# Kernel tuning notes

Measured on AMD Instinct MI355X. Metric: run time of the kernel, lower is better.

## Reference

```python
import jax, jax.numpy as jnp
import numpy as np

N = 100000   # n_node
D = 100      # emb_size
K = 100      # K1 (channel 0 cluster count)
L = 3        # layers
NNZ = 1600000  # sparse adjacency nnz (avg degree 16)


def _l2norm(x):
    # F.normalize(x, dim=-1, p=2) with eps=1e-12
    return x / jnp.maximum(jnp.linalg.norm(x, axis=-1, keepdims=True), 1e-12)


def setup_inputs() -> dict:
    key = jax.random.key(0)
    ks = jax.random.split(key, 8)
    s = 1.0 / np.sqrt(D)  # module's uniform(-stdv, stdv) init
    embedding = jax.random.normal(ks[0], (N, D), jnp.float32)
    adj = jax.random.uniform(ks[1], (N,), jnp.float32) + 0.01  # per-node positive weights
    edge_rows = jax.random.randint(ks[2], (NNZ,), 0, N, jnp.int32)
    edge_cols = jax.random.randint(ks[3], (NNZ,), 0, N, jnp.int32)
    edge_vals = jax.random.uniform(ks[4], (NNZ,), jnp.float32)
    W_item = jax.random.uniform(ks[5], (L, D, D), jnp.float32, -s, s)
    W_i1 = jax.random.uniform(ks[6], (D, D), jnp.float32, -s, s)
    W_i2 = jax.random.uniform(ks[7], (D, K), jnp.float32, -s, s)
    return {"embedding": embedding, "adj": adj, "edge_vals": edge_vals,
            "W_item": W_item, "W_i1": W_i1, "W_i2": W_i2,
            "edge_rows": edge_rows, "edge_cols": edge_cols}


def reference(embedding, adj, edge_vals, W_item, W_i1, W_i2, edge_rows, edge_cols):
    # ItemConv.forward for one channel (channel=0), adjacency as COO sparse [N,N]
    def spmm(x):  # torch.sparse.mm(adjacency, x)
        return jax.ops.segment_sum(edge_vals[:, None] * x[edge_cols], edge_rows,
                                   num_segments=N)

    x = embedding
    final = [x]
    finalh = []
    for i in range(L):
        x = x @ W_item[i]                       # Linear(D, D, bias=False)
        x = spmm(x)                             # [N, D]
        H1 = jax.nn.relu(x @ W_i1 + x)          # residual + ReLU
        H1 = jax.nn.softmax(H1 @ W_i2, axis=1)  # [N, K] soft cluster assignment
        h = H1.T * adj[None, :]                 # [K, N]
        h = h / jnp.sum(h, axis=0)              # column-normalize over clusters
        h = h @ x                               # [K, D] cluster aggregates
        h = H1 @ h                              # [N, D] redistribute to nodes
        x = h + x                               # residual
        final.append(_l2norm(x))
        finalh.append(_l2norm(h))
    item_embeddings = sum(final) / (L + 1)
    hs = sum(finalh) / L
    return item_embeddings, hs
```

## Files before the change

### kernel.cpp

```cpp
#include <hip/hip_runtime.h>
#include <hip/hip_bf16.h>

#define D 100
#define XS 128

typedef __hip_bfloat16 bf16;
typedef __attribute__((ext_vector_type(8))) short bf16x8;
typedef __attribute__((ext_vector_type(4))) float f32x4;

__device__ __forceinline__ float ldf(const void* p, long long i, int f32) {
    return f32 ? ((const float*)p)[i] : __bfloat162float(((const bf16*)p)[i]);
}

__device__ __forceinline__ float b2f(unsigned short u) {
    return __uint_as_float(((unsigned int)u) << 16);
}

__device__ __forceinline__ unsigned short f2bu(float x) {
    union { bf16 b; unsigned short u; } cv;
    cv.b = __float2bfloat16(x);
    return cv.u;
}

__global__ void detectk(const void* __restrict__ emb, int* __restrict__ flag)
{
    const unsigned short* u = (const unsigned short*)emb;
    __shared__ int cnt;
    if (threadIdx.x == 0) cnt = 0;
    __syncthreads();
    int good = 0;
    for (int i = threadIdx.x; i < 512; i += 256) {
        int e = (u[i] >> 7) & 0xFF;
        if (e >= 118 && e <= 137) good++;
    }
    atomicAdd(&cnt, good);
    __syncthreads();
    if (threadIdx.x == 0) *flag = (cnt >= 410) ? 0 : 1;
}


__global__ void wprep(const void* __restrict__ wi, const void* __restrict__ w1,
    const void* __restrict__ w2, const int* __restrict__ flag,
    bf16* __restrict__ wh, bf16* __restrict__ wl)
{
    int i = blockIdx.x * 256 + threadIdx.x;
    if (i >= 5 * 112 * 128) return;
    int m = i / (112 * 128), rem = i - m * (112 * 128);
    int c = rem / 128, k = rem - c * 128;
    float w = 0.f;
    if (c < D && k < D) {
        int f = *flag;
        long long si = (long long)k * D + c;
        if (m < 3)       w = ldf(wi, m * 10000 + si, f);
        else if (m == 3) w = ldf(w1, si, f);
        else             w = ldf(w2, si, f);
    }
    bf16 hb = __float2bfloat16(w);
    wh[i] = hb;
    wl[i] = __float2bfloat16(w - __bfloat162float(hb));
}


__global__ void hsm_conv(const float* __restrict__ hsm, bf16* __restrict__ hh,
    bf16* __restrict__ hl)
{
    int i = blockIdx.x * 256 + threadIdx.x;
    if (i >= 112 * 128) return;
    int c = i / 128, k = i - c * 128;
    float w = (c < D && k < D) ? hsm[k * D + c] : 0.f;
    bf16 hb = __float2bfloat16(w);
    hh[i] = hb;
    hl[i] = __float2bfloat16(w - __bfloat162float(hb));
}

__global__ void initk(const void* __restrict__ emb, const int* __restrict__ flag,
    bf16* __restrict__ x, float* __restrict__ o0, float* __restrict__ o1, int n)
{
    long long i = (long long)blockIdx.x * 256 + threadIdx.x;
    if (i >= (long long)n * XS) return;
    int nn = (int)(i >> 7), d = (int)(i & 127);
    float v = 0.f;
    if (d < D) v = ldf(emb, (long long)nn * D + d, *flag);
    x[i] = __float2bfloat16(v);
    if (d < D) {
        o0[(long long)nn * D + d] = v * 0.25f;
        o1[(long long)nn * D + d] = 0.0f;
    }
}


template<int MODE>
__global__ __launch_bounds__(64) void gemm_mfma(
    const bf16* __restrict__ X, const bf16* __restrict__ Wh,
    const bf16* __restrict__ Wl, bf16* __restrict__ Y, int n,
    const bf16* __restrict__ X2, float* __restrict__ o0, float* __restrict__ o1)
{
    const int lane = threadIdx.x;
    const int r16 = lane & 15, kg = lane >> 4;
    const long long m0 = (long long)blockIdx.x * 64;

    f32x4 acc[4][7];
    #pragma unroll
    for (int i = 0; i < 4; ++i)
        #pragma unroll
        for (int j = 0; j < 7; ++j) acc[i][j] = (f32x4){0.f, 0.f, 0.f, 0.f};

    const bf16* xa = X + (m0 + r16) * XS + kg * 8;
    #pragma unroll
    for (int ks = 0; ks < 4; ++ks) {
        bf16x8 a0 = *(const bf16x8*)(xa + ks * 32);
        bf16x8 a1 = *(const bf16x8*)(xa + 16 * XS + ks * 32);
        bf16x8 a2 = *(const bf16x8*)(xa + 32 * XS + ks * 32);
        bf16x8 a3 = *(const bf16x8*)(xa + 48 * XS + ks * 32);
        #pragma unroll
        for (int nt = 0; nt < 7; ++nt) {
            const bf16* wb = Wh + (nt * 16 + r16) * 128 + ks * 32 + kg * 8;
            bf16x8 bh = *(const bf16x8*)wb;
            bf16x8 bl = *(const bf16x8*)(wb + (Wl - Wh));
            acc[0][nt] = __builtin_amdgcn_mfma_f32_16x16x32_bf16(a0, bh, acc[0][nt], 0, 0, 0);
            acc[0][nt] = __builtin_amdgcn_mfma_f32_16x16x32_bf16(a0, bl, acc[0][nt], 0, 0, 0);
            acc[1][nt] = __builtin_amdgcn_mfma_f32_16x16x32_bf16(a1, bh, acc[1][nt], 0, 0, 0);
            acc[1][nt] = __builtin_amdgcn_mfma_f32_16x16x32_bf16(a1, bl, acc[1][nt], 0, 0, 0);
            acc[2][nt] = __builtin_amdgcn_mfma_f32_16x16x32_bf16(a2, bh, acc[2][nt], 0, 0, 0);
            acc[2][nt] = __builtin_amdgcn_mfma_f32_16x16x32_bf16(a2, bl, acc[2][nt], 0, 0, 0);
            acc[3][nt] = __builtin_amdgcn_mfma_f32_16x16x32_bf16(a3, bh, acc[3][nt], 0, 0, 0);
            acc[3][nt] = __builtin_amdgcn_mfma_f32_16x16x32_bf16(a3, bl, acc[3][nt], 0, 0, 0);
        }
    }

    if (MODE == 0 || MODE == 1) {
        #pragma unroll
        for (int rt = 0; rt < 4; ++rt)
            #pragma unroll
            for (int nt = 0; nt < 7; ++nt) {
                int col = nt * 16 + r16;
                #pragma unroll
                for (int r = 0; r < 4; ++r) {
                    long long row = m0 + rt * 16 + kg * 4 + r;
                    if (row >= n) continue;
                    float v = acc[rt][nt][r];
                    if (MODE == 1) {
                        v += __bfloat162float(X[row * XS + col]);
                        v = fmaxf(v, 0.f);
                    }
                    Y[row * XS + col] = __float2bfloat16(v);
                }
            }
    } else if (MODE == 2) {
        const bool v6 = (r16 < 4);
        #pragma unroll
        for (int rt = 0; rt < 4; ++rt)
            #pragma unroll
            for (int r = 0; r < 4; ++r) {
                float m = -3.0e38f;
                #pragma unroll
                for (int nt = 0; nt < 7; ++nt)
                    if (nt < 6 || v6) m = fmaxf(m, acc[rt][nt][r]);
                m = fmaxf(m, __shfl_xor(m, 1));
                m = fmaxf(m, __shfl_xor(m, 2));
                m = fmaxf(m, __shfl_xor(m, 4));
                m = fmaxf(m, __shfl_xor(m, 8));
                float ex[7]; float s = 0.f;
                #pragma unroll
                for (int nt = 0; nt < 7; ++nt) {
                    ex[nt] = (nt < 6 || v6) ? __expf(acc[rt][nt][r] - m) : 0.f;
                    s += ex[nt];
                }
                s += __shfl_xor(s, 1);
                s += __shfl_xor(s, 2);
                s += __shfl_xor(s, 4);
                s += __shfl_xor(s, 8);
                float inv = 1.f / s;
                long long row = m0 + rt * 16 + kg * 4 + r;
                if (row < n) {
                    #pragma unroll
                    for (int nt = 0; nt < 7; ++nt)
                        Y[row * XS + nt * 16 + r16] = __float2bfloat16(ex[nt] * inv);
                }
            }
    } else {
        #pragma unroll
        for (int rt = 0; rt < 4; ++rt)
            #pragma unroll
            for (int r = 0; r < 4; ++r) {
                long long row = m0 + rt * 16 + kg * 4 + r;
                float xn[7], hn[7];
                float sx = 0.f, sh2 = 0.f;
                #pragma unroll
                for (int nt = 0; nt < 7; ++nt) {
                    int col = nt * 16 + r16;
                    float h = acc[rt][nt][r];
                    float x2v = __bfloat162float(X2[row * XS + col]);
                    float xv = h + x2v;
                    xn[nt] = xv; hn[nt] = h;
                    sx += xv * xv; sh2 += h * h;
                }
                sx  += __shfl_xor(sx, 1);  sx  += __shfl_xor(sx, 2);
                sx  += __shfl_xor(sx, 4);  sx  += __shfl_xor(sx, 8);
                sh2 += __shfl_xor(sh2, 1); sh2 += __shfl_xor(sh2, 2);
                sh2 += __shfl_xor(sh2, 4); sh2 += __shfl_xor(sh2, 8);
                float ia = 0.25f        / fmaxf(sqrtf(sx), 1e-12f);
                float ib = (1.f / 3.f)  / fmaxf(sqrtf(sh2), 1e-12f);
                if (row < n) {
                    long long bo = row * D;
                    #pragma unroll
                    for (int nt = 0; nt < 7; ++nt) {
                        int col = nt * 16 + r16;
                        Y[row * XS + col] = __float2bfloat16(xn[nt]);
                        if (col < D) {
                            o0[bo + col] += xn[nt] * ia;
                            o1[bo + col] += hn[nt] * ib;
                        }
                    }
                }
            }
    }

    {
        long long row = m0 + lane;
        if (row < n) {
            *(int4*)(Y + row * XS + 112) = make_int4(0, 0, 0, 0);
            *(int4*)(Y + row * XS + 120) = make_int4(0, 0, 0, 0);
        }
    }
}


__global__ void hist(const int* __restrict__ rows, const int* __restrict__ cols,
    int* __restrict__ cnt, int n, int nnz)
{
    int e = blockIdx.x * 256 + threadIdx.x;
    if (e >= nnz) return;
    int r = rows[e], c = cols[e];
    if ((unsigned)r >= (unsigned)n || (unsigned)c >= (unsigned)n) return;
    atomicAdd(&cnt[r], 1);
}

__global__ void scan1(const int* __restrict__ cnt, int* __restrict__ offs,
    int* __restrict__ bsum, int n)
{
    __shared__ int sh[256];
    int b = blockIdx.x, t = threadIdx.x;
    int base = b * 2048 + t * 8;
    int v[8];
    int s = 0;
    #pragma unroll
    for (int i = 0; i < 8; ++i) {
        int idx = base + i;
        v[i] = (idx < n) ? cnt[idx] : 0;
        s += v[i];
    }
    sh[t] = s; __syncthreads();
    for (int off = 1; off < 256; off <<= 1) {
        int x = (t >= off) ? sh[t - off] : 0;
        __syncthreads();
        sh[t] += x;
        __syncthreads();
    }
    int run = sh[t] - s;
    #pragma unroll
    for (int i = 0; i < 8; ++i) {
        run += v[i];
        int idx = base + i;
        if (idx < n) offs[idx + 1] = run;
    }
    if (t == 255) bsum[b] = sh[255];
}

__global__ void scan2(int* __restrict__ bsum, int nb)
{
    __shared__ int sh[256];
    int t = threadIdx.x;
    int v = (t < nb) ? bsum[t] : 0;
    sh[t] = v; __syncthreads();
    for (int off = 1; off < 256; off <<= 1) {
        int x = (t >= off) ? sh[t - off] : 0;
        __syncthreads();
        sh[t] += x;
        __syncthreads();
    }
    if (t < nb) bsum[t] = sh[t] - v;
}

__global__ void scan3(int* __restrict__ offs, const int* __restrict__ bsum, int n)
{
    int i = blockIdx.x * 256 + threadIdx.x;
    if (i == 0) offs[0] = 0;
    if (i < n) offs[i + 1] += bsum[i >> 11];
}

__global__ void scatter(const int* __restrict__ rows, const int* __restrict__ cols,
    const void* __restrict__ vals, const int* __restrict__ flag,
    const int* __restrict__ offs, int* __restrict__ fill, int2* __restrict__ ecv,
    int n, int nnz)
{
    int e = blockIdx.x * 256 + threadIdx.x;
    if (e >= nnz) return;
    int r = rows[e], c = cols[e];
    if ((unsigned)r >= (unsigned)n || (unsigned)c >= (unsigned)n) return;
    int pos = offs[r] + atomicAdd(&fill[r], 1);
    float v = ldf(vals, e, *flag);
    ecv[pos] = make_int2(c, __float_as_int(v));
}


__global__ void spmm_csr(const int* __restrict__ offs, const int2* __restrict__ ecv,
    const bf16* __restrict__ X, bf16* __restrict__ Y, int n)
{
    int wid = (int)(((long long)blockIdx.x * 256 + threadIdx.x) >> 6);
    int lane = threadIdx.x & 63;
    if (wid >= n) return;
    int s = offs[wid], e = offs[wid + 1];
    int d0 = lane * 2;
    if (d0 >= D) return;
    float a0 = 0.f, a1 = 0.f;
    int j = s;
    for (; j + 7 < e; j += 8) {
        int2 cv[8];
        unsigned int u[8];
        #pragma unroll
        for (int q = 0; q < 8; ++q) cv[q] = ecv[j + q];
        #pragma unroll
        for (int q = 0; q < 8; ++q)
            u[q] = *(const unsigned int*)(X + (long long)cv[q].x * XS + d0);
        #pragma unroll
        for (int q = 0; q < 8; ++q) {
            float v = __int_as_float(cv[q].y);
            a0 = fmaf(v, b2f((unsigned short)u[q]), a0);
            a1 = fmaf(v, b2f((unsigned short)(u[q] >> 16)), a1);
        }
    }
    for (; j < e; ++j) {
        int2 cv = ecv[j];
        unsigned int u = *(const unsigned int*)(X + (long long)cv.x * XS + d0);
        float v = __int_as_float(cv.y);
        a0 = fmaf(v, b2f((unsigned short)u), a0);
        a1 = fmaf(v, b2f((unsigned short)(u >> 16)), a1);
    }
    *(unsigned int*)(Y + (long long)wid * XS + d0) =
        ((unsigned int)f2bu(a1) << 16) | f2bu(a0);
}


#define HSM_G 512
#define HSM_BATCH 32

__global__ void hsm_partial(const bf16* __restrict__ H1, const bf16* __restrict__ X2,
    float* __restrict__ partials, int n)
{
    __shared__ float sh[HSM_BATCH][D];
    __shared__ float sx[HSM_BATCH][D];
    const int t = threadIdx.x;
    const int tk = t / 10;
    const int td = t - tk * 10;

    float acc[4][10];
    #pragma unroll
    for (int i = 0; i < 4; ++i)
        #pragma unroll
        for (int j = 0; j < 10; ++j) acc[i][j] = 0.f;

    const int per = (n + HSM_G - 1) / HSM_G;
    const int s = blockIdx.x * per;
    int e = s + per; if (e > n) e = n;

    for (int base = s; base < e; base += HSM_BATCH) {
        int cnt = e - base; if (cnt > HSM_BATCH) cnt = HSM_BATCH;
        __syncthreads();
        for (int v = t; v < cnt * 25; v += 256) {
            int r = v / 25, c4 = v - (v / 25) * 25;
            ushort4 h4 = *(const ushort4*)(H1 + (long long)(base + r) * XS + 4 * c4);
            ushort4 x4 = *(const ushort4*)(X2 + (long long)(base + r) * XS + 4 * c4);
            sh[r][4 * c4 + 0] = b2f(h4.x);
            sh[r][4 * c4 + 1] = b2f(h4.y);
            sh[r][4 * c4 + 2] = b2f(h4.z);
            sh[r][4 * c4 + 3] = b2f(h4.w);
            sx[r][4 * c4 + 0] = b2f(x4.x);
            sx[r][4 * c4 + 1] = b2f(x4.y);
            sx[r][4 * c4 + 2] = b2f(x4.z);
            sx[r][4 * c4 + 3] = b2f(x4.w);
        }
        __syncthreads();
        if (t < 250) {
            #pragma unroll 8
            for (int r = 0; r < cnt; ++r) {
                float4 a = *(const float4*)&sh[r][tk * 4];
                const float2* bp = (const float2*)&sx[r][td * 10];
                float2 b0 = bp[0], b1 = bp[1], b2 = bp[2], b3 = bp[3], b4 = bp[4];
                float b[10] = {b0.x, b0.y, b1.x, b1.y, b2.x, b2.y, b3.x, b3.y, b4.x, b4.y};
                #pragma unroll
                for (int j = 0; j < 10; ++j) {
                    acc[0][j] = fmaf(a.x, b[j], acc[0][j]);
                    acc[1][j] = fmaf(a.y, b[j], acc[1][j]);
                    acc[2][j] = fmaf(a.z, b[j], acc[2][j]);
                    acc[3][j] = fmaf(a.w, b[j], acc[3][j]);
                }
            }
        }
    }

    if (t < 250) {
        float* out = partials + (long long)blockIdx.x * (D * D);
        #pragma unroll
        for (int i = 0; i < 4; ++i)
            #pragma unroll
            for (int j = 0; j < 10; ++j)
                out[(tk * 4 + i) * D + td * 10 + j] = acc[i][j];
    }
}

__global__ void hsm_reduce(const float* __restrict__ partials, float* __restrict__ hsm)
{
    int i = blockIdx.x * 256 + threadIdx.x;
    if (i >= D * D) return;
    float s0 = 0.f, s1 = 0.f;
    for (int b = 0; b < HSM_G; b += 2) {
        s0 += partials[(long long)b * (D * D) + i];
        s1 += partials[(long long)(b + 1) * (D * D) + i];
    }
    hsm[i] = s0 + s1;
}


extern "C" void kernel_launch(void* const* d_in, const int* in_sizes, int n_in,
                              void* d_out, int out_size, void* d_ws, size_t ws_size,
                              hipStream_t stream)
{
    const void* emb   = d_in[0];
    const void* evals = d_in[2];
    const void* Wit   = d_in[3];
    const void* Wi1   = d_in[4];
    const void* Wi2   = d_in[5];
    const int* erows  = (const int*)d_in[6];
    const int* ecols  = (const int*)d_in[7];
    const int N   = in_sizes[0] / D;
    const int NNZ = in_sizes[2];
    const long long ND = (long long)N * D;
    const size_t NB = (size_t)N * XS * 2;

    float* o0 = (float*)d_out;
    float* o1 = o0 + ND;

    char* base = (char*)d_ws;
    size_t off = 0;
    auto alloc = [&](size_t bytes) -> void* {
        void* r = base + off;
        off += (bytes + 255) & ~(size_t)255;
        return r;
    };
    int*   flag  = (int*)  alloc(256);
    float* hsm   = (float*)alloc(D * D * 4);
    bf16*  WH    = (bf16*) alloc(5 * 112 * 128 * 2);
    bf16*  WL    = (bf16*) alloc(5 * 112 * 128 * 2);
    bf16*  hsmTh = (bf16*) alloc(112 * 128 * 2);
    bf16*  hsmTl = (bf16*) alloc(112 * 128 * 2);
    int*   offs  = (int*)  alloc(((size_t)N + 1) * 4);
    int*   cnt   = (int*)  alloc((size_t)N * 4);
    int*   bsum  = (int*)  alloc(1024);
    int2*  ecv   = (int2*) alloc((size_t)NNZ * 8);
    bf16*  B1    = (bf16*) alloc(NB);
    bf16*  B2    = (bf16*) alloc(NB);
    bf16*  H1    = (bf16*) alloc(NB);
    (void)alloc(64 * XS * 2);
    float* partials = (float*)B2;

    const int gND = (int)((ND + 255) / 256);
    const int gNX = (int)(((long long)N * XS + 255) / 256);
    const int gE  = (NNZ + 255) / 256;
    const int nb  = (N + 2047) / 2048;
    const int gM  = (N + 63) / 64;
    const int gS  = (N + 3) / 4;

    detectk<<<1, 256, 0, stream>>>(emb, flag);
    wprep<<<(5 * 112 * 128 + 255) / 256, 256, 0, stream>>>(Wit, Wi1, Wi2, flag, WH, WL);
    initk<<<gNX, 256, 0, stream>>>(emb, flag, B1, o0, o1, N);

    hipMemsetAsync(cnt, 0, (size_t)N * 4, stream);
    hist<<<gE, 256, 0, stream>>>(erows, ecols, cnt, N, NNZ);
    scan1<<<nb, 256, 0, stream>>>(cnt, offs, bsum, N);
    scan2<<<1, 256, 0, stream>>>(bsum, nb);
    scan3<<<(N + 255) / 256, 256, 0, stream>>>(offs, bsum, N);
    hipMemsetAsync(cnt, 0, (size_t)N * 4, stream);
    scatter<<<gE, 256, 0, stream>>>(erows, ecols, evals, flag, offs, cnt, ecv, N, NNZ);

    for (int l = 0; l < 3; ++l) {
        gemm_mfma<0><<<gM, 64, 0, stream>>>(B1, WH + l * 14336, WL + l * 14336,
                                            B2, N, nullptr, nullptr, nullptr);
        spmm_csr<<<gS, 256, 0, stream>>>(offs, ecv, B2, B1, N);
        gemm_mfma<1><<<gM, 64, 0, stream>>>(B1, WH + 3 * 14336, WL + 3 * 14336,
                                            B2, N, nullptr, nullptr, nullptr);
        gemm_mfma<2><<<gM, 64, 0, stream>>>(B2, WH + 4 * 14336, WL + 4 * 14336,
                                            H1, N, nullptr, nullptr, nullptr);
        hsm_partial<<<HSM_G, 256, 0, stream>>>(H1, B1, partials, N);
        hsm_reduce<<<(D * D + 255) / 256, 256, 0, stream>>>(partials, hsm);
        hsm_conv<<<(112 * 128 + 255) / 256, 256, 0, stream>>>(hsm, hsmTh, hsmTl);
        gemm_mfma<3><<<gM, 64, 0, stream>>>(H1, hsmTh, hsmTl, B1, N, B1, o0, o1);
    }
}
```

Before: 1.279 ms.

## Fuse chained GEMMs through LDS tiles and merge hsm reduce with conversion

Merges the residual+ReLU GEMM with the softmax cluster GEMM by staging the intermediate in an LDS tile. The hsm redistribution GEMM is chained with the next layer's W_item GEMM, so B1/B2 round trips to HBM are avoided. It also folds the hsm reduce and transpose/split conversion into one kernel, and switches to 256-thread blocks with 32 rows per wave. This cuts kernel launches and global traffic on 100k-row bf16 buffers, at the cost of more LDS use and smaller per-wave row tiles with less reuse of the weight loads.

```diff
diff --git a/kernel.cpp b/kernel.cpp
--- a/kernel.cpp
+++ b/kernel.cpp
@@ -60,19 +60,6 @@
     wl[i] = __float2bfloat16(w - __bfloat162float(hb));
 }
 
-
-__global__ void hsm_conv(const float* __restrict__ hsm, bf16* __restrict__ hh,
-    bf16* __restrict__ hl)
-{
-    int i = blockIdx.x * 256 + threadIdx.x;
-    if (i >= 112 * 128) return;
-    int c = i / 128, k = i - c * 128;
-    float w = (c < D && k < D) ? hsm[k * D + c] : 0.f;
-    bf16 hb = __float2bfloat16(w);
-    hh[i] = hb;
-    hl[i] = __float2bfloat16(w - __bfloat162float(hb));
-}
-
 __global__ void initk(const void* __restrict__ emb, const int* __restrict__ flag,
     bf16* __restrict__ x, float* __restrict__ o0, float* __restrict__ o1, int n)
 {
@@ -89,139 +76,252 @@
 }
 
 
-template<int MODE>
-__global__ __launch_bounds__(64) void gemm_mfma(
+#define MFMA_K_LOOP(XPTR, WHP, WLP, ACC)                                          \
+    {                                                                             \
+        const bf16* xa_ = (XPTR);                                                 \
+        _Pragma("unroll")                                                         \
+        for (int ks = 0; ks < 4; ++ks) {                                          \
+            bf16x8 a0 = *(const bf16x8*)(xa_ + ks * 32);                          \
+            bf16x8 a1 = *(const bf16x8*)(xa_ + 16 * XS + ks * 32);                \
+            _Pragma("unroll")                                                     \
+            for (int nt = 0; nt < 7; ++nt) {                                      \
+                const bf16* wb = (WHP) + (nt * 16 + r16) * 128 + ks * 32 + kg * 8;\
+                bf16x8 bh = *(const bf16x8*)wb;                                   \
+                bf16x8 bl = *(const bf16x8*)(wb + ((WLP) - (WHP)));               \
+                ACC[0][nt] = __builtin_amdgcn_mfma_f32_16x16x32_bf16(a0, bh, ACC[0][nt], 0, 0, 0); \
+                ACC[0][nt] = __builtin_amdgcn_mfma_f32_16x16x32_bf16(a0, bl, ACC[0][nt], 0, 0, 0); \
+                ACC[1][nt] = __builtin_amdgcn_mfma_f32_16x16x32_bf16(a1, bh, ACC[1][nt], 0, 0, 0); \
+                ACC[1][nt] = __builtin_amdgcn_mfma_f32_16x16x32_bf16(a1, bl, ACC[1][nt], 0, 0, 0); \
+            }                                                                     \
+        }                                                                         \
+    }
+
+__global__ __launch_bounds__(256) void gemm0(
     const bf16* __restrict__ X, const bf16* __restrict__ Wh,
-    const bf16* __restrict__ Wl, bf16* __restrict__ Y, int n,
-    const bf16* __restrict__ X2, float* __restrict__ o0, float* __restrict__ o1)
-{
-    const int lane = threadIdx.x;
+    const bf16* __restrict__ Wl, bf16* __restrict__ Y, int n)
+{
+    const int wave = threadIdx.x >> 6, lane = threadIdx.x & 63;
     const int r16 = lane & 15, kg = lane >> 4;
-    const long long m0 = (long long)blockIdx.x * 64;
-
-    f32x4 acc[4][7];
-    #pragma unroll
-    for (int i = 0; i < 4; ++i)
+    const long long m0 = ((long long)blockIdx.x * 4 + wave) * 32;
+
+    f32x4 acc[2][7];
+    #pragma unroll
+    for (int i = 0; i < 2; ++i)
         #pragma unroll
         for (int j = 0; j < 7; ++j) acc[i][j] = (f32x4){0.f, 0.f, 0.f, 0.f};
 
-    const bf16* xa = X + (m0 + r16) * XS + kg * 8;
+    MFMA_K_LOOP(X + (m0 + r16) * XS + kg * 8, Wh, Wl, acc);
+
+    #pragma unroll
+    for (int rt = 0; rt < 2; ++rt)
+        #pragma unroll
+        for (int nt = 0; nt < 7; ++nt) {
+            int col = nt * 16 + r16;
+            #pragma unroll
+            for (int r = 0; r < 4; ++r) {
+                long long row = m0 + rt * 16 + kg * 4 + r;
+                if (row < n) Y[row * XS + col] = __float2bfloat16(acc[rt][nt][r]);
+            }
+        }
+}
+
+__global__ __launch_bounds__(256) void gemm12(
+    const bf16* __restrict__ X,
+    const bf16* __restrict__ W1h, const bf16* __restrict__ W1l,
+    const bf16* __restrict__ W2h, const bf16* __restrict__ W2l,
+    bf16* __restrict__ H1, int n)
+{
+    __shared__ ushort tile[4][32][136];
+    const int wave = threadIdx.x >> 6, lane = threadIdx.x & 63;
+    const int r16 = lane & 15, kg = lane >> 4;
+    const long long m0 = ((long long)blockIdx.x * 4 + wave) * 32;
+
+    f32x4 acc[2][7];
+    #pragma unroll
+    for (int i = 0; i < 2; ++i)
+        #pragma unroll
+        for (int j = 0; j < 7; ++j) acc[i][j] = (f32x4){0.f, 0.f, 0.f, 0.f};
+
+    MFMA_K_LOOP(X + (m0 + r16) * XS + kg * 8, W1h, W1l, acc);
+
+    #pragma unroll
+    for (int rt = 0; rt < 2; ++rt)
+        #pragma unroll
+        for (int nt = 0; nt < 7; ++nt) {
+            int col = nt * 16 + r16;
+            #pragma unroll
+            for (int r = 0; r < 4; ++r) {
+                long long row = m0 + rt * 16 + kg * 4 + r;
+                float v = acc[rt][nt][r] + __bfloat162float(X[row * XS + col]);
+                tile[wave][rt * 16 + kg * 4 + r][col] = f2bu(fmaxf(v, 0.f));
+            }
+        }
+    {
+        int rr = lane >> 1, half = lane & 1;
+        *(int4*)&tile[wave][rr][112 + half * 8] = make_int4(0, 0, 0, 0);
+    }
+
+    f32x4 ac2[2][7];
+    #pragma unroll
+    for (int i = 0; i < 2; ++i)
+        #pragma unroll
+        for (int j = 0; j < 7; ++j) ac2[i][j] = (f32x4){0.f, 0.f, 0.f, 0.f};
+
     #pragma unroll
     for (int ks = 0; ks < 4; ++ks) {
-        bf16x8 a0 = *(const bf16x8*)(xa + ks * 32);
-        bf16x8 a1 = *(const bf16x8*)(xa + 16 * XS + ks * 32);
-        bf16x8 a2 = *(const bf16x8*)(xa + 32 * XS + ks * 32);
-        bf16x8 a3 = *(const bf16x8*)(xa + 48 * XS + ks * 32);
+        bf16x8 a0 = *(const bf16x8*)&tile[wave][r16][ks * 32 + kg * 8];
+        bf16x8 a1 = *(const bf16x8*)&tile[wave][16 + r16][ks * 32 + kg * 8];
         #pragma unroll
         for (int nt = 0; nt < 7; ++nt) {
-            const bf16* wb = Wh + (nt * 16 + r16) * 128 + ks * 32 + kg * 8;
+            const bf16* wb = W2h + (nt * 16 + r16) * 128 + ks * 32 + kg * 8;
             bf16x8 bh = *(const bf16x8*)wb;
-            bf16x8 bl = *(const bf16x8*)(wb + (Wl - Wh));
-            acc[0][nt] = __builtin_amdgcn_mfma_f32_16x16x32_bf16(a0, bh, acc[0][nt], 0, 0, 0);
-            acc[0][nt] = __builtin_amdgcn_mfma_f32_16x16x32_bf16(a0, bl, acc[0][nt], 0, 0, 0);
-            acc[1][nt] = __builtin_amdgcn_mfma_f32_16x16x32_bf16(a1, bh, acc[1][nt], 0, 0, 0);
-            acc[1][nt] = __builtin_amdgcn_mfma_f32_16x16x32_bf16(a1, bl, acc[1][nt], 0, 0, 0);
-            acc[2][nt] = __builtin_amdgcn_mfma_f32_16x16x32_bf16(a2, bh, acc[2][nt], 0, 0, 0);
-            acc[2][nt] = __builtin_amdgcn_mfma_f32_16x16x32_bf16(a2, bl, acc[2][nt], 0, 0, 0);
-            acc[3][nt] = __builtin_amdgcn_mfma_f32_16x16x32_bf16(a3, bh, acc[3][nt], 0, 0, 0);
-            acc[3][nt] = __builtin_amdgcn_mfma_f32_16x16x32_bf16(a3, bl, acc[3][nt], 0, 0, 0);
-        }
-    }
-
-    if (MODE == 0 || MODE == 1) {
-        #pragma unroll
-        for (int rt = 0; rt < 4; ++rt)
+            bf16x8 bl = *(const bf16x8*)(wb + (W2l - W2h));
+            ac2[0][nt] = __builtin_amdgcn_mfma_f32_16x16x32_bf16(a0, bh, ac2[0][nt], 0, 0, 0);
+            ac2[0][nt] = __builtin_amdgcn_mfma_f32_16x16x32_bf16(a0, bl, ac2[0][nt], 0, 0, 0);
+            ac2[1][nt] = __builtin_amdgcn_mfma_f32_16x16x32_bf16(a1, bh, ac2[1][nt], 0, 0, 0);
+            ac2[1][nt] = __builtin_amdgcn_mfma_f32_16x16x32_bf16(a1, bl, ac2[1][nt], 0, 0, 0);
+        }
+    }
+
+    const bool v6 = (r16 < 4);
+    #pragma unroll
+    for (int rt = 0; rt < 2; ++rt)
+        #pragma unroll
+        for (int r = 0; r < 4; ++r) {
+            float m = -3.0e38f;
+            #pragma unroll
+            for (int nt = 0; nt < 7; ++nt)
+                if (nt < 6 || v6) m = fmaxf(m, ac2[rt][nt][r]);
+            m = fmaxf(m, __shfl_xor(m, 1));
+            m = fmaxf(m, __shfl_xor(m, 2));
+            m = fmaxf(m, __shfl_xor(m, 4));
+            m = fmaxf(m, __shfl_xor(m, 8));
+            float ex[7]; float s = 0.f;
+            #pragma unroll
+            for (int nt = 0; nt < 7; ++nt) {
+                ex[nt] = (nt < 6 || v6) ? __expf(ac2[rt][nt][r] - m) : 0.f;
+                s += ex[nt];
+            }
+            s += __shfl_xor(s, 1);
+            s += __shfl_xor(s, 2);
+            s += __shfl_xor(s, 4);
+            s += __shfl_xor(s, 8);
+            float inv = 1.f / s;
+            long long row = m0 + rt * 16 + kg * 4 + r;
+            if (row < n) {
+                #pragma unroll
+                for (int nt = 0; nt < 7; ++nt)
+                    H1[row * XS + nt * 16 + r16] = __float2bfloat16(ex[nt] * inv);
+            }
+        }
+    {
+        int rr = lane >> 1, half = lane & 1;
+        long long row = m0 + rr;
+        if (row < n)
+            *(int4*)(H1 + row * XS + 112 + half * 8) = make_int4(0, 0, 0, 0);
+    }
+}
+
+template<int CHAIN>
+__global__ __launch_bounds__(256) void gemm30(
+    const bf16* __restrict__ H1,
+    const bf16* __restrict__ Hh, const bf16* __restrict__ Hl,
+    const bf16* __restrict__ X2,
+    const bf16* __restrict__ Wnh, const bf16* __restrict__ Wnl,
+    bf16* __restrict__ B2out, int n,
+    float* __restrict__ o0, float* __restrict__ o1)
+{
+    __shared__ ushort tile[CHAIN ? 4 : 1][32][136];
+    const int wave = threadIdx.x >> 6, lane = threadIdx.x & 63;
+    const int r16 = lane & 15, kg = lane >> 4;
+    const long long m0 = ((long long)blockIdx.x * 4 + wave) * 32;
+
+    f32x4 acc[2][7];
+    #pragma unroll
+    for (int i = 0; i < 2; ++i)
+        #pragma unroll
+        for (int j = 0; j < 7; ++j) acc[i][j] = (f32x4){0.f, 0.f, 0.f, 0.f};
+
+    MFMA_K_LOOP(H1 + (m0 + r16) * XS + kg * 8, Hh, Hl, acc);
+
+    #pragma unroll
+    for (int rt = 0; rt < 2; ++rt)
+        #pragma unroll
+        for (int r = 0; r < 4; ++r) {
+            long long row = m0 + rt * 16 + kg * 4 + r;
+            float xn[7], hn[7];
+            float sx = 0.f, sh2 = 0.f;
+            #pragma unroll
+            for (int nt = 0; nt < 7; ++nt) {
+                int col = nt * 16 + r16;
+                float h = acc[rt][nt][r];
+                float x2v = __bfloat162float(X2[row * XS + col]);
+                float xv = h + x2v;
+                xn[nt] = xv; hn[nt] = h;
+                sx += xv * xv; sh2 += h * h;
+            }
+            sx  += __shfl_xor(sx, 1);  sx  += __shfl_xor(sx, 2);
+            sx  += __shfl_xor(sx, 4);  sx  += __shfl_xor(sx, 8);
+            sh2 += __shfl_xor(sh2, 1); sh2 += __shfl_xor(sh2, 2);
+            sh2 += __shfl_xor(sh2, 4); sh2 += __shfl_xor(sh2, 8);
+            float ia = 0.25f       / fmaxf(sqrtf(sx), 1e-12f);
+            float ib = (1.f / 3.f) / fmaxf(sqrtf(sh2), 1e-12f);
+            if (row < n) {
+                long long bo = row * D;
+                #pragma unroll
+                for (int nt = 0; nt < 7; ++nt) {
+                    int col = nt * 16 + r16;
+                    if (col < D) {
+                        o0[bo + col] += xn[nt] * ia;
+                        o1[bo + col] += hn[nt] * ib;
+                    }
+                }
+            }
+            if (CHAIN) {
+                #pragma unroll
+                for (int nt = 0; nt < 7; ++nt)
+                    tile[wave][rt * 16 + kg * 4 + r][nt * 16 + r16] = f2bu(xn[nt]);
+            }
+        }
+
+    if (CHAIN) {
+        {
+            int rr = lane >> 1, half = lane & 1;
+            *(int4*)&tile[wave][rr][112 + half * 8] = make_int4(0, 0, 0, 0);
+        }
+        f32x4 ac2[2][7];
+        #pragma unroll
+        for (int i = 0; i < 2; ++i)
+            #pragma unroll
+            for (int j = 0; j < 7; ++j) ac2[i][j] = (f32x4){0.f, 0.f, 0.f, 0.f};
+
+        #pragma unroll
+        for (int ks = 0; ks < 4; ++ks) {
+            bf16x8 a0 = *(const bf16x8*)&tile[wave][r16][ks * 32 + kg * 8];
+            bf16x8 a1 = *(const bf16x8*)&tile[wave][16 + r16][ks * 32 + kg * 8];
+            #pragma unroll
+            for (int nt = 0; nt < 7; ++nt) {
+                const bf16* wb = Wnh + (nt * 16 + r16) * 128 + ks * 32 + kg * 8;
+                bf16x8 bh = *(const bf16x8*)wb;
+                bf16x8 bl = *(const bf16x8*)(wb + (Wnl - Wnh));
+                ac2[0][nt] = __builtin_amdgcn_mfma_f32_16x16x32_bf16(a0, bh, ac2[0][nt], 0, 0, 0);
+                ac2[0][nt] = __builtin_amdgcn_mfma_f32_16x16x32_bf16(a0, bl, ac2[0][nt], 0, 0, 0);
+                ac2[1][nt] = __builtin_amdgcn_mfma_f32_16x16x32_bf16(a1, bh, ac2[1][nt], 0, 0, 0);
+                ac2[1][nt] = __builtin_amdgcn_mfma_f32_16x16x32_bf16(a1, bl, ac2[1][nt], 0, 0, 0);
+            }
+        }
+        #pragma unroll
+        for (int rt = 0; rt < 2; ++rt)
             #pragma unroll
             for (int nt = 0; nt < 7; ++nt) {
                 int col = nt * 16 + r16;
                 #pragma unroll
                 for (int r = 0; r < 4; ++r) {
                     long long row = m0 + rt * 16 + kg * 4 + r;
-                    if (row >= n) continue;
-                    float v = acc[rt][nt][r];
-                    if (MODE == 1) {
-                        v += __bfloat162float(X[row * XS + col]);
-                        v = fmaxf(v, 0.f);
-                    }
-                    Y[row * XS + col] = __float2bfloat16(v);
+                    if (row < n)
+                        B2out[row * XS + col] = __float2bfloat16(ac2[rt][nt][r]);
                 }
             }
-    } else if (MODE == 2) {
-        const bool v6 = (r16 < 4);
-        #pragma unroll
-        for (int rt = 0; rt < 4; ++rt)
-            #pragma unroll
-            for (int r = 0; r < 4; ++r) {
-                float m = -3.0e38f;
-                #pragma unroll
-                for (int nt = 0; nt < 7; ++nt)
-                    if (nt < 6 || v6) m = fmaxf(m, acc[rt][nt][r]);
-                m = fmaxf(m, __shfl_xor(m, 1));
-                m = fmaxf(m, __shfl_xor(m, 2));
-                m = fmaxf(m, __shfl_xor(m, 4));
-                m = fmaxf(m, __shfl_xor(m, 8));
-                float ex[7]; float s = 0.f;
-                #pragma unroll
-                for (int nt = 0; nt < 7; ++nt) {
-                    ex[nt] = (nt < 6 || v6) ? __expf(acc[rt][nt][r] - m) : 0.f;
-                    s += ex[nt];
-                }
-                s += __shfl_xor(s, 1);
-                s += __shfl_xor(s, 2);
-                s += __shfl_xor(s, 4);
-                s += __shfl_xor(s, 8);
-                float inv = 1.f / s;
-                long long row = m0 + rt * 16 + kg * 4 + r;
-                if (row < n) {
-                    #pragma unroll
-                    for (int nt = 0; nt < 7; ++nt)
-                        Y[row * XS + nt * 16 + r16] = __float2bfloat16(ex[nt] * inv);
-                }
-            }
-    } else {
-        #pragma unroll
-        for (int rt = 0; rt < 4; ++rt)
-            #pragma unroll
-            for (int r = 0; r < 4; ++r) {
-                long long row = m0 + rt * 16 + kg * 4 + r;
-                float xn[7], hn[7];
-                float sx = 0.f, sh2 = 0.f;
-                #pragma unroll
-                for (int nt = 0; nt < 7; ++nt) {
-                    int col = nt * 16 + r16;
-                    float h = acc[rt][nt][r];
-                    float x2v = __bfloat162float(X2[row * XS + col]);
-                    float xv = h + x2v;
-                    xn[nt] = xv; hn[nt] = h;
-                    sx += xv * xv; sh2 += h * h;
-                }
-                sx  += __shfl_xor(sx, 1);  sx  += __shfl_xor(sx, 2);
-                sx  += __shfl_xor(sx, 4);  sx  += __shfl_xor(sx, 8);
-                sh2 += __shfl_xor(sh2, 1); sh2 += __shfl_xor(sh2, 2);
-                sh2 += __shfl_xor(sh2, 4); sh2 += __shfl_xor(sh2, 8);
-                float ia = 0.25f        / fmaxf(sqrtf(sx), 1e-12f);
-                float ib = (1.f / 3.f)  / fmaxf(sqrtf(sh2), 1e-12f);
-                if (row < n) {
-                    long long bo = row * D;
-                    #pragma unroll
-                    for (int nt = 0; nt < 7; ++nt) {
-                        int col = nt * 16 + r16;
-                        Y[row * XS + col] = __float2bfloat16(xn[nt]);
-                        if (col < D) {
-                            o0[bo + col] += xn[nt] * ia;
-                            o1[bo + col] += hn[nt] * ib;
-                        }
-                    }
-                }
-            }
-    }
-
-    {
-        long long row = m0 + lane;
-        if (row < n) {
-            *(int4*)(Y + row * XS + 112) = make_int4(0, 0, 0, 0);
-            *(int4*)(Y + row * XS + 120) = make_int4(0, 0, 0, 0);
-        }
     }
 }
 
@@ -405,20 +505,29 @@
         for (int i = 0; i < 4; ++i)
             #pragma unroll
             for (int j = 0; j < 10; ++j)
-                out[(tk * 4 + i) * D + td * 10 + j] = acc[i][j];
-    }
-}
-
-__global__ void hsm_reduce(const float* __restrict__ partials, float* __restrict__ hsm)
+                out[(td * 10 + j) * D + (tk * 4 + i)] = acc[i][j];
+    }
+}
+
+__global__ void hsm_rc(const float* __restrict__ P, bf16* __restrict__ hh,
+    bf16* __restrict__ hl)
 {
     int i = blockIdx.x * 256 + threadIdx.x;
-    if (i >= D * D) return;
-    float s0 = 0.f, s1 = 0.f;
-    for (int b = 0; b < HSM_G; b += 2) {
-        s0 += partials[(long long)b * (D * D) + i];
-        s1 += partials[(long long)(b + 1) * (D * D) + i];
-    }
-    hsm[i] = s0 + s1;
+    if (i >= 112 * 128) return;
+    int c = i >> 7, k = i & 127;
+    float w = 0.f;
+    if (c < D && k < D) {
+        const float* p = P + c * D + k;
+        float s0 = 0.f, s1 = 0.f;
+        for (int b = 0; b < HSM_G; b += 2) {
+            s0 += p[(long long)b * (D * D)];
+            s1 += p[(long long)(b + 1) * (D * D)];
+        }
+        w = s0 + s1;
+    }
+    bf16 hb = __float2bfloat16(w);
+    hh[i] = hb;
+    hl[i] = __float2bfloat16(w - __bfloat162float(hb));
 }
 
 
@@ -449,7 +558,6 @@
         return r;
     };
     int*   flag  = (int*)  alloc(256);
-    float* hsm   = (float*)alloc(D * D * 4);
     bf16*  WH    = (bf16*) alloc(5 * 112 * 128 * 2);
     bf16*  WL    = (bf16*) alloc(5 * 112 * 128 * 2);
     bf16*  hsmTh = (bf16*) alloc(112 * 128 * 2);
@@ -461,14 +569,13 @@
     bf16*  B1    = (bf16*) alloc(NB);
     bf16*  B2    = (bf16*) alloc(NB);
     bf16*  H1    = (bf16*) alloc(NB);
-    (void)alloc(64 * XS * 2);
+    (void)alloc(128 * XS * 2);
     float* partials = (float*)B2;
 
-    const int gND = (int)((ND + 255) / 256);
     const int gNX = (int)(((long long)N * XS + 255) / 256);
     const int gE  = (NNZ + 255) / 256;
     const int nb  = (N + 2047) / 2048;
-    const int gM  = (N + 63) / 64;
+    const int gM  = (N + 127) / 128;
     const int gS  = (N + 3) / 4;
 
     detectk<<<1, 256, 0, stream>>>(emb, flag);
@@ -483,17 +590,19 @@
     hipMemsetAsync(cnt, 0, (size_t)N * 4, stream);
     scatter<<<gE, 256, 0, stream>>>(erows, ecols, evals, flag, offs, cnt, ecv, N, NNZ);
 
+    gemm0<<<gM, 256, 0, stream>>>(B1, WH, WL, B2, N);
+
     for (int l = 0; l < 3; ++l) {
-        gemm_mfma<0><<<gM, 64, 0, stream>>>(B1, WH + l * 14336, WL + l * 14336,
-                                            B2, N, nullptr, nullptr, nullptr);
         spmm_csr<<<gS, 256, 0, stream>>>(offs, ecv, B2, B1, N);
-        gemm_mfma<1><<<gM, 64, 0, stream>>>(B1, WH + 3 * 14336, WL + 3 * 14336,
-                                            B2, N, nullptr, nullptr, nullptr);
-        gemm_mfma<2><<<gM, 64, 0, stream>>>(B2, WH + 4 * 14336, WL + 4 * 14336,
-                                            H1, N, nullptr, nullptr, nullptr);
+        gemm12<<<gM, 256, 0, stream>>>(B1, WH + 3 * 14336, WL + 3 * 14336,
+                                       WH + 4 * 14336, WL + 4 * 14336, H1, N);
         hsm_partial<<<HSM_G, 256, 0, stream>>>(H1, B1, partials, N);
-        hsm_reduce<<<(D * D + 255) / 256, 256, 0, stream>>>(partials, hsm);
-        hsm_conv<<<(112 * 128 + 255) / 256, 256, 0, stream>>>(hsm, hsmTh, hsmTl);
-        gemm_mfma<3><<<gM, 64, 0, stream>>>(H1, hsmTh, hsmTl, B1, N, B1, o0, o1);
-    }
-}
+        hsm_rc<<<(112 * 128 + 255) / 256, 256, 0, stream>>>(partials, hsmTh, hsmTl);
+        if (l < 2)
+            gemm30<1><<<gM, 256, 0, stream>>>(H1, hsmTh, hsmTl, B1,
+                WH + (l + 1) * 14336, WL + (l + 1) * 14336, B2, N, o0, o1);
+        else
+            gemm30<0><<<gM, 256, 0, stream>>>(H1, hsmTh, hsmTl, B1,
+                nullptr, nullptr, nullptr, N, o0, o1);
+    }
+}
```

After: 1.343 ms. 5.0% more time.
